# Performance work log

Hardware: AMD Instinct MI355X
Metric: run time of the kernel (lower is better)

## Reference

```python
import jax, jax.numpy as jnp
import numpy as np

H = 512      # hidden_dim
OPS = 12     # num_ops
E = 112      # total_edges = num_cells * sum(i+2 for i in range(num_nodes)) = 8*14


def setup_inputs() -> dict:
    key = jax.random.key(0)
    ks = jax.random.split(key, 16)
    s = lambda k, shape: jax.random.normal(k, shape, dtype=jnp.float32) * 0.05
    return {
        "temperature": 1,
        "h0": s(ks[0], (2, H)),
        "c0": s(ks[1], (2, H)),
        "Wih0": s(ks[2], (4 * H, H)),
        "Whh0": s(ks[3], (4 * H, H)),
        "bih0": s(ks[4], (4 * H,)),
        "bhh0": s(ks[5], (4 * H,)),
        "Wih1": s(ks[6], (4 * H, H)),
        "Whh1": s(ks[7], (4 * H, H)),
        "bih1": s(ks[8], (4 * H,)),
        "bhh1": s(ks[9], (4 * H,)),
        "emb": s(ks[10], (OPS, H)),
        "cW1": s(ks[11], (E, H, H)),
        "cb1": s(ks[12], (E, H)),
        "cW2": s(ks[13], (E, H, OPS)),
        "cb2": s(ks[14], (E, OPS)),
    }


def _lstm_cell(x, h, c, Wih, Whh, bih, bhh):
    # PyTorch LSTM gate order: i, f, g, o
    gates = x @ Wih.T + bih + h @ Whh.T + bhh  # [4H]
    i, f, g, o = jnp.split(gates, 4)
    c2 = jax.nn.sigmoid(f) * c + jax.nn.sigmoid(i) * jnp.tanh(g)
    h2 = jax.nn.sigmoid(o) * jnp.tanh(c2)
    return h2, c2


def reference(temperature, h0, c0, Wih0, Whh0, bih0, bhh0,
              Wih1, Whh1, bih1, bhh1, emb, cW1, cb1, cW2, cb2):
    temp = jnp.asarray(temperature, jnp.float32)
    # Gumbel-max trick == torch Categorical sampling (fixed on-device noise)
    gumbel = jax.random.gumbel(jax.random.key(42), (E, OPS), dtype=jnp.float32)

    def step(carry, xs):
        h, c, prev_action = carry          # h, c: [2, H]
        idx, W1, b1, W2, b2, gnoise = xs
        x = jnp.where(idx == 0, jnp.zeros((H,), jnp.float32), emb[prev_action])
        h0n, c0n = _lstm_cell(x, h[0], c[0], Wih0, Whh0, bih0, bhh0)
        h1n, c1n = _lstm_cell(h0n, h[1], c[1], Wih1, Whh1, bih1, bhh1)
        hmlp = jax.nn.relu(h1n @ W1 + b1)   # controller hidden
        logits = (hmlp @ W2 + b2) / temp    # [OPS]
        logp = jax.nn.log_softmax(logits)
        action = jnp.argmax(logits + gnoise).astype(jnp.int32)
        lp = logp[action]
        ent = -jnp.sum(jnp.exp(logp) * logp)
        new_carry = (jnp.stack([h0n, h1n]), jnp.stack([c0n, c1n]), action)
        return new_carry, (action, lp, ent)

    init = (h0, c0, jnp.int32(0))
    xs = (jnp.arange(E), cW1, cb1, cW2, cb2, gumbel)
    _, (actions, log_probs, entropies) = jax.lax.scan(step, init, xs)
    return actions, log_probs, entropies
```

## Files before the change

### kernel.cpp

```cpp
#include <hip/hip_runtime.h>
#include <math.h>

#define H    512
#define OPS  12
#define E    112
#define NWG  128
#define NT   256

typedef unsigned long long u64;

#define TW_BASE  16
#define TW_HB0   0
#define TW_HB1   1024
#define TW_HMB   2048
#define TW_TOTAL 3072

__device__ __forceinline__ float sigf(float x) { return 1.f / (1.f + expf(-x)); }

__device__ __forceinline__ void threefry_42(unsigned x0, unsigned x1,
                                            unsigned& o0, unsigned& o1) {
  const unsigned k0 = 0u, k1 = 42u;
  const unsigned k2 = k0 ^ k1 ^ 0x1BD11BDAu;
  x0 += k0; x1 += k1;
#define TF_R(rot) { x0 += x1; x1 = (x1 << rot) | (x1 >> (32 - rot)); x1 ^= x0; }
  TF_R(13) TF_R(15) TF_R(26) TF_R(6)
  x0 += k1; x1 += k2 + 1u;
  TF_R(17) TF_R(29) TF_R(16) TF_R(24)
  x0 += k2; x1 += k0 + 2u;
  TF_R(13) TF_R(15) TF_R(26) TF_R(6)
  x0 += k0; x1 += k1 + 3u;
  TF_R(17) TF_R(29) TF_R(16) TF_R(24)
  x0 += k1; x1 += k2 + 4u;
  TF_R(13) TF_R(15) TF_R(26) TF_R(6)
  x0 += k2; x1 += k0 + 5u;
#undef TF_R
  o0 = x0; o1 = x1;
}

__device__ __forceinline__ float bits_to_gumbel(unsigned bits) {
  unsigned fb = (bits >> 9) | 0x3f800000u;
  float u = __uint_as_float(fb) - 1.0f;
  u = u + 1.17549435e-38f;
  u = fmaxf(1.17549435e-38f, u);
  return -logf(-logf(u));
}

__device__ __forceinline__ float decode_temp(const void* temp_p) {
  float tf = *(const float*)temp_p;
  float a = fabsf(tf);
  if (a > 1e-6f && a < 1e6f) return tf;
  int ti = *(const int*)temp_p;
  if (ti != 0 && ti > -1000000 && ti < 1000000) return (float)ti;
  double td = *(const double*)temp_p;
  double ad = fabs(td);
  if (ad > 1e-6 && ad < 1e6) return (float)td;
  return 1.0f;
}

__device__ __forceinline__ void tag_store(u64* p, unsigned tag, float f) {
  u64 v = ((u64)tag << 32) | (u64)__float_as_uint(f);
  __hip_atomic_store(p, v, __ATOMIC_RELAXED, __HIP_MEMORY_SCOPE_SYSTEM);
}
__device__ __forceinline__ float tag_poll(const u64* p, unsigned tag) {
  u64 v = __hip_atomic_load(p, __ATOMIC_RELAXED, __HIP_MEMORY_SCOPE_SYSTEM);
  while ((unsigned)(v >> 32) != tag) {
    __builtin_amdgcn_s_sleep(1);
    v = __hip_atomic_load(p, __ATOMIC_RELAXED, __HIP_MEMORY_SCOPE_SYSTEM);
  }
  return __uint_as_float((unsigned)v);
}

__global__ void k_init(u64* tw) {
  int t = blockIdx.x * blockDim.x + threadIdx.x;
  if (t < TW_TOTAL) tw[t] = 0ull;
}
__global__ void k_diag(float* out, float v) {
  if (threadIdx.x == 0 && blockIdx.x == 0) out[0] = v;
}

__global__ void __launch_bounds__(NT)
policy_persist(const void* temp_p,
               const float* __restrict__ h0_in, const float* __restrict__ c0_in,
               const float* __restrict__ Wih0,  const float* __restrict__ Whh0,
               const float* __restrict__ bih0,  const float* __restrict__ bhh0,
               const float* __restrict__ Wih1,  const float* __restrict__ Whh1,
               const float* __restrict__ bih1,  const float* __restrict__ bhh1,
               const float* __restrict__ emb,   const float* __restrict__ cW1,
               const float* __restrict__ cb1,   const float* __restrict__ cW2,
               const float* __restrict__ cb2,
               float* __restrict__ out, float* ws) {
  __shared__ __align__(16) float shp0[H], shp1[H], hm[H];
  __shared__ float g0pre[16], g1bpre[16], g1loc[16];
  __shared__ float ewloc[12 * 16], b0loc[16], b1loc[16];
  __shared__ float gum[E * OPS];
  __shared__ float w1s[512 * 5];
  __shared__ float w2s[512 * 13];
  __shared__ float c0loc[4], c1loc[4];
  __shared__ float spart[4][4];
  __shared__ int s_act;

  const int tid = threadIdx.x;
  const int bid = blockIdx.x;
  const int j0  = bid * 4;
  const int cb  = (bid & 7) * 16 + (bid >> 3);
  const float invt = 1.f / decode_temp(temp_p);

  u64* HB0 = (u64*)(ws + TW_BASE) + TW_HB0;
  u64* HB1 = (u64*)(ws + TW_BASE) + TW_HB1;
  u64* HMB = (u64*)(ws + TW_BASE) + TW_HMB;

  for (int p = tid; p < E * OPS; p += NT) {
    unsigned y0, y1;
    threefry_42(0u, (unsigned)p, y0, y1);
    gum[p] = bits_to_gumbel(y0 ^ y1);
  }
  for (int j = tid; j < H; j += NT) {
    shp0[j] = h0_in[j];
    shp1[j] = h0_in[H + j];
  }
  if (tid < 192) {
    int a = tid / 16, ridx = tid % 16;
    int g = ridx >> 2, dj = ridx & 3;
    int row = g * H + j0 + dj;
    const float* er = emb + a * H;
    const float* wr = Wih0 + (size_t)row * H;
    float acc = 0.f;
    for (int k = 0; k < H; k += 4) {
      float4 e4 = *(const float4*)(er + k);
      float4 w4 = *(const float4*)(wr + k);
      acc += e4.x * w4.x + e4.y * w4.y + e4.z * w4.z + e4.w * w4.w;
    }
    ewloc[tid] = acc;
  }
  if (tid < 16) {
    int g = tid >> 2, dj = tid & 3;
    int row = g * H + j0 + dj;
    b0loc[tid] = bih0[row] + bhh0[row];
    b1loc[tid] = bih1[row] + bhh1[row];
  }
  if (tid < 4) {
    c0loc[tid] = c0_in[j0 + tid];
    c1loc[tid] = c0_in[H + j0 + tid];
  }
  __syncthreads();

  {
    int rowidx = tid >> 3, lane = tid & 7;
    int cell = rowidx >> 4, ridx = rowidx & 15;
    int g = ridx >> 2, dj = ridx & 3;
    int row = g * H + j0 + dj;
    const float* wr = (cell ? Whh1 : Whh0) + (size_t)row * H + lane * 64;
    const float* hv = (cell ? shp1 : shp0) + lane * 64;
    float acc = 0.f;
#pragma unroll
    for (int k = 0; k < 64; k += 4) {
      float4 w4 = *(const float4*)(wr + k);
      acc += w4.x * hv[k] + w4.y * hv[k + 1] + w4.z * hv[k + 2] + w4.w * hv[k + 3];
    }
    acc += __shfl_xor(acc, 1);
    acc += __shfl_xor(acc, 2);
    acc += __shfl_xor(acc, 4);
    if (lane == 0) {
      if (cell == 0) g0pre[ridx] = acc + b0loc[ridx];
      else           g1bpre[ridx] = acc;
    }
    const float* wb = cW1 + (size_t)cb * 4;
    float4 r0 = *(const float4*)(wb + (size_t)tid * H);
    float4 r1 = *(const float4*)(wb + (size_t)(tid + 256) * H);
    int k0 = tid * 5, k1 = (tid + 256) * 5;
    w1s[k0] = r0.x; w1s[k0 + 1] = r0.y; w1s[k0 + 2] = r0.z; w1s[k0 + 3] = r0.w;
    w1s[k1] = r1.x; w1s[k1 + 1] = r1.y; w1s[k1 + 2] = r1.z; w1s[k1 + 3] = r1.w;
  }
  __syncthreads();

#pragma unroll 1
  for (int i = 0; i < E; ++i) {
    const int p = i & 1;
    const unsigned tg = (unsigned)(i + 1);

    if (i > 0) {
      const int q = (i - 1) & 1;
      const unsigned tgp = (unsigned)i;
      int t2 = tid * 2;
      hm[t2]     = tag_poll(&HMB[q * 512 + t2],     tgp);
      hm[t2 + 1] = tag_poll(&HMB[q * 512 + t2 + 1], tgp);
      __syncthreads();
      if (tid < 64) {
        float lg[OPS];
#pragma unroll
        for (int o = 0; o < OPS; ++o) lg[o] = 0.f;
#pragma unroll
        for (int jj = 0; jj < 8; ++jj) {
          int j = jj * 64 + tid;
          float hmv = hm[j];
          const float* w2r = &w2s[j * 13];
#pragma unroll
          for (int o = 0; o < OPS; ++o) lg[o] += hmv * w2r[o];
        }
#pragma unroll
        for (int s = 1; s < 64; s <<= 1) {
#pragma unroll
          for (int o = 0; o < OPS; ++o) lg[o] += __shfl_xor(lg[o], s);
        }
#pragma unroll
        for (int o = 0; o < OPS; ++o) lg[o] = (lg[o] + cb2[(i - 1) * OPS + o]) * invt;
        float mx = lg[0];
#pragma unroll
        for (int o = 1; o < OPS; ++o) mx = fmaxf(mx, lg[o]);
        float se = 0.f;
#pragma unroll
        for (int o = 0; o < OPS; ++o) se += expf(lg[o] - mx);
        float logZ = mx + logf(se);
        float best = -1e30f; int act = 0;
#pragma unroll
        for (int o = 0; o < OPS; ++o) {
          float v = lg[o] + gum[(i - 1) * OPS + o];
          if (v > best) { best = v; act = o; }
        }
        if (tid == 0) {
          s_act = act;
          if (bid == 0) {
            float lp = lg[act] - logZ;
            float ent = 0.f;
            for (int o = 0; o < OPS; ++o) {
              float l2 = lg[o] - logZ;
              ent -= expf(l2) * l2;
            }
            out[i - 1]         = (float)act;
            out[E + i - 1]     = lp;
            out[2 * E + i - 1] = ent;
          }
        }
      }
    }

    if (tid < 4) {
      int a = (i > 0) ? s_act : -1;
      float gi = g0pre[tid];
      float gf = g0pre[4 + tid];
      float gg = g0pre[8 + tid];
      float go = g0pre[12 + tid];
      if (a >= 0) {
        gi += ewloc[a * 16 + tid];
        gf += ewloc[a * 16 + 4 + tid];
        gg += ewloc[a * 16 + 8 + tid];
        go += ewloc[a * 16 + 12 + tid];
      }
      float cn = sigf(gf) * c0loc[tid] + sigf(gi) * tanhf(gg);
      c0loc[tid] = cn;
      tag_store(&HB0[p * 512 + j0 + tid], tg, sigf(go) * tanhf(cn));
    }

    {
      int t2 = tid * 2;
      shp0[t2]     = tag_poll(&HB0[p * 512 + t2],     tg);
      shp0[t2 + 1] = tag_poll(&HB0[p * 512 + t2 + 1], tg);
    }
    __syncthreads();

    {
      int ridx = tid >> 4, lane = tid & 15;
      int g = ridx >> 2, dj = ridx & 3;
      int row = g * H + j0 + dj;
      const float* wr = Wih1 + (size_t)row * H + lane * 32;
      const float* hv = shp0 + lane * 32;
      float acc = 0.f;
#pragma unroll
      for (int k = 0; k < 32; k += 4) {
        float4 w4 = *(const float4*)(wr + k);
        acc += w4.x * hv[k] + w4.y * hv[k + 1] + w4.z * hv[k + 2] + w4.w * hv[k + 3];
      }
      acc += __shfl_xor(acc, 1);
      acc += __shfl_xor(acc, 2);
      acc += __shfl_xor(acc, 4);
      acc += __shfl_xor(acc, 8);
      if (lane == 0) g1loc[ridx] = acc + g1bpre[ridx] + b1loc[ridx];
    }
    __syncthreads();

    if (tid < 4) {
      float gi = g1loc[tid];
      float gf = g1loc[4 + tid];
      float gg = g1loc[8 + tid];
      float go = g1loc[12 + tid];
      float cn = sigf(gf) * c1loc[tid] + sigf(gi) * tanhf(gg);
      c1loc[tid] = cn;
      tag_store(&HB1[p * 512 + j0 + tid], tg, sigf(go) * tanhf(cn));
    }

    {
      int t2 = tid * 2;
      shp1[t2]     = tag_poll(&HB1[p * 512 + t2],     tg);
      shp1[t2 + 1] = tag_poll(&HB1[p * 512 + t2 + 1], tg);
    }
    __syncthreads();

    {
      int wv = tid >> 6, ln = tid & 63;
      int jl = ln & 3, ks = ln >> 2;
      int kbase = wv * 128 + ks * 8;
      float acc = 0.f;
#pragma unroll
      for (int t = 0; t < 8; ++t) {
        int k = kbase + t;
        acc += shp1[k] * w1s[k * 5 + jl];
      }
      acc += __shfl_xor(acc, 4);
      acc += __shfl_xor(acc, 8);
      acc += __shfl_xor(acc, 16);
      acc += __shfl_xor(acc, 32);
      if (ln < 4) spart[wv][ln] = acc;
    }
    __syncthreads();
    if (tid < 4) {
      float s = spart[0][tid] + spart[1][tid] + spart[2][tid] + spart[3][tid];
      s += cb1[(size_t)i * H + cb * 4 + tid];
      tag_store(&HMB[p * 512 + cb * 4 + tid], tg, fmaxf(s, 0.f));
    }

    {
      const float* wsrc = cW2 + (size_t)i * H * OPS;
#pragma unroll
      for (int r = 0; r < 6; ++r) {
        int q = tid + 256 * r;
        float4 v = *(const float4*)(wsrc + 4 * q);
        int f = 4 * q;
        w2s[(f / 12) * 13 + (f % 12)]             = v.x;
        w2s[((f + 1) / 12) * 13 + ((f + 1) % 12)] = v.y;
        w2s[((f + 2) / 12) * 13 + ((f + 2) % 12)] = v.z;
        w2s[((f + 3) / 12) * 13 + ((f + 3) % 12)] = v.w;
      }
    }
    if (i + 1 < E) {
      const float* wb = cW1 + (size_t)(i + 1) * H * H + (size_t)cb * 4;
      float4 r0 = *(const float4*)(wb + (size_t)tid * H);
      float4 r1 = *(const float4*)(wb + (size_t)(tid + 256) * H);
      {
        int rowidx = tid >> 3, lane = tid & 7;
        int cell = rowidx >> 4, ridx = rowidx & 15;
        int g = ridx >> 2, dj = ridx & 3;
        int row = g * H + j0 + dj;
        const float* wr = (cell ? Whh1 : Whh0) + (size_t)row * H + lane * 64;
        const float* hv = (cell ? shp1 : shp0) + lane * 64;
        float acc = 0.f;
#pragma unroll
        for (int k = 0; k < 64; k += 4) {
          float4 w4 = *(const float4*)(wr + k);
          acc += w4.x * hv[k] + w4.y * hv[k + 1] + w4.z * hv[k + 2] + w4.w * hv[k + 3];
        }
        acc += __shfl_xor(acc, 1);
        acc += __shfl_xor(acc, 2);
        acc += __shfl_xor(acc, 4);
        if (lane == 0) {
          if (cell == 0) g0pre[ridx] = acc + b0loc[ridx];
          else           g1bpre[ridx] = acc;
        }
      }
      int k0 = tid * 5, k1 = (tid + 256) * 5;
      w1s[k0] = r0.x; w1s[k0 + 1] = r0.y; w1s[k0 + 2] = r0.z; w1s[k0 + 3] = r0.w;
      w1s[k1] = r1.x; w1s[k1 + 1] = r1.y; w1s[k1 + 2] = r1.z; w1s[k1 + 3] = r1.w;
    }
    __syncthreads();
  }

  if (bid == 0) {
    const int q = (E - 1) & 1;
    int t2 = tid * 2;
    hm[t2]     = tag_poll(&HMB[q * 512 + t2],     (unsigned)E);
    hm[t2 + 1] = tag_poll(&HMB[q * 512 + t2 + 1], (unsigned)E);
    __syncthreads();
    if (tid < 64) {
      float lg[OPS];
#pragma unroll
      for (int o = 0; o < OPS; ++o) lg[o] = 0.f;
#pragma unroll
      for (int jj = 0; jj < 8; ++jj) {
        int j = jj * 64 + tid;
        float hmv = hm[j];
        const float* w2r = &w2s[j * 13];
#pragma unroll
        for (int o = 0; o < OPS; ++o) lg[o] += hmv * w2r[o];
      }
#pragma unroll
      for (int s = 1; s < 64; s <<= 1) {
#pragma unroll
        for (int o = 0; o < OPS; ++o) lg[o] += __shfl_xor(lg[o], s);
      }
#pragma unroll
      for (int o = 0; o < OPS; ++o) lg[o] = (lg[o] + cb2[(E - 1) * OPS + o]) * invt;
      float mx = lg[0];
#pragma unroll
      for (int o = 1; o < OPS; ++o) mx = fmaxf(mx, lg[o]);
      float se = 0.f;
#pragma unroll
      for (int o = 0; o < OPS; ++o) se += expf(lg[o] - mx);
      float logZ = mx + logf(se);
      float best = -1e30f; int act = 0;
#pragma unroll
      for (int o = 0; o < OPS; ++o) {
        float v = lg[o] + gum[(E - 1) * OPS + o];
        if (v > best) { best = v; act = o; }
      }
      if (tid == 0) {
        float lp = lg[act] - logZ;
        float ent = 0.f;
        for (int o = 0; o < OPS; ++o) {
          float l2 = lg[o] - logZ;
          ent -= expf(l2) * l2;
        }
        out[E - 1]     = (float)act;
        out[2 * E - 1] = lp;
        out[3 * E - 1] = ent;
      }
    }
  }
}

extern "C" void kernel_launch(void* const* d_in, const int* in_sizes, int n_in,
                              void* d_out, int out_size, void* d_ws, size_t ws_size,
                              hipStream_t stream) {
  (void)out_size; (void)ws_size;
  float* out = (float*)d_out;
  float* ws  = (float*)d_ws;

  (void)hipGetLastError();

  static const long long expect[16] = {
      1, 1024, 1024, 1048576, 1048576, 2048, 2048,
      1048576, 1048576, 2048, 2048, 6144,
      29360128, 57344, 688128, 1344 };
  int bad = -1;
  if (n_in != 16) bad = 99;
  else {
    for (int i = 0; i < 16; ++i)
      if ((long long)in_sizes[i] != expect[i]) { bad = i; break; }
  }

  k_init<<<12, 256, 0, stream>>>((u64*)(ws + TW_BASE));
  if (bad >= 0) {
    k_diag<<<1, 64, 0, stream>>>(out, 80000.0f + (float)bad);
    return;
  }

  policy_persist<<<NWG, NT, 0, stream>>>(
      d_in[0],
      (const float*)d_in[1],  (const float*)d_in[2],
      (const float*)d_in[3],  (const float*)d_in[4],
      (const float*)d_in[5],  (const float*)d_in[6],
      (const float*)d_in[7],  (const float*)d_in[8],
      (const float*)d_in[9],  (const float*)d_in[10],
      (const float*)d_in[11], (const float*)d_in[12],
      (const float*)d_in[13], (const float*)d_in[14],
      (const float*)d_in[15],
      out, ws);

  hipError_t e = hipGetLastError();
  if (e != hipSuccess) {
    k_diag<<<1, 64, 0, stream>>>(out, 90000.0f + (float)(int)e);
  }
}
```

Baseline: 1.074 ms.

## Speculate layer-0 LSTM output for all actions to remove a grid barrier per step

Layer 0 of the LSTM now runs one step ahead and speculatively for all 12 possible previous actions. Each block publishes 12 candidate h0 slices, gathers the full speculative h0 vectors, and precomputes the Wih1 contributions for every action. Once the sampled action is known, the matching h0, c0 and layer-1 input term are picked, which removes one global tag-polled exchange (HB0) from the serial critical path of each step. In exchange it does 12x the layer-0 gate and Wih1 work, polls a 12x larger exchange buffer, and uses much more shared memory. It also merges the paired tag polls into a single loop.

Result: slower. 3.097 ms (+188.4%).

```diff
diff --git a/kernel.cpp b/kernel.cpp
--- a/kernel.cpp
+++ b/kernel.cpp
@@ -9,11 +9,10 @@
 
 typedef unsigned long long u64;
 
-#define TW_BASE  16
-#define TW_HB0   0
-#define TW_HB1   1024
-#define TW_HMB   2048
-#define TW_TOTAL 3072
+#define TW_HB1   0
+#define TW_HMB   1024
+#define TW_SPEC  2048
+#define TW_TOTAL (2048 + 2 * 6144)
 
 __device__ __forceinline__ float sigf(float x) { return 1.f / (1.f + expf(-x)); }
 
@@ -61,13 +60,17 @@
   u64 v = ((u64)tag << 32) | (u64)__float_as_uint(f);
   __hip_atomic_store(p, v, __ATOMIC_RELAXED, __HIP_MEMORY_SCOPE_SYSTEM);
 }
-__device__ __forceinline__ float tag_poll(const u64* p, unsigned tag) {
-  u64 v = __hip_atomic_load(p, __ATOMIC_RELAXED, __HIP_MEMORY_SCOPE_SYSTEM);
-  while ((unsigned)(v >> 32) != tag) {
+__device__ __forceinline__ void tag_poll2(const u64* p0, const u64* p1,
+                                          unsigned tag, float& f0, float& f1) {
+  u64 a = __hip_atomic_load(p0, __ATOMIC_RELAXED, __HIP_MEMORY_SCOPE_SYSTEM);
+  u64 b = __hip_atomic_load(p1, __ATOMIC_RELAXED, __HIP_MEMORY_SCOPE_SYSTEM);
+  while (((unsigned)(a >> 32) != tag) || ((unsigned)(b >> 32) != tag)) {
     __builtin_amdgcn_s_sleep(1);
-    v = __hip_atomic_load(p, __ATOMIC_RELAXED, __HIP_MEMORY_SCOPE_SYSTEM);
-  }
-  return __uint_as_float((unsigned)v);
+    a = __hip_atomic_load(p0, __ATOMIC_RELAXED, __HIP_MEMORY_SCOPE_SYSTEM);
+    b = __hip_atomic_load(p1, __ATOMIC_RELAXED, __HIP_MEMORY_SCOPE_SYSTEM);
+  }
+  f0 = __uint_as_float((unsigned)a);
+  f1 = __uint_as_float((unsigned)b);
 }
 
 __global__ void k_init(u64* tw) {
@@ -89,8 +92,10 @@
                const float* __restrict__ cb1,   const float* __restrict__ cW2,
                const float* __restrict__ cb2,
                float* __restrict__ out, float* ws) {
-  __shared__ __align__(16) float shp0[H], shp1[H], hm[H];
+  __shared__ __align__(16) float h0full[H], shp1[H], hm[H];
+  __shared__ __align__(16) float h0specfull[12 * H];
   __shared__ float g0pre[16], g1bpre[16], g1loc[16];
+  __shared__ float G1Aspec[12 * 16], c0spec[12 * 4];
   __shared__ float ewloc[12 * 16], b0loc[16], b1loc[16];
   __shared__ float gum[E * OPS];
   __shared__ float w1s[512 * 5];
@@ -105,9 +110,9 @@
   const int cb  = (bid & 7) * 16 + (bid >> 3);
   const float invt = 1.f / decode_temp(temp_p);
 
-  u64* HB0 = (u64*)(ws + TW_BASE) + TW_HB0;
-  u64* HB1 = (u64*)(ws + TW_BASE) + TW_HB1;
-  u64* HMB = (u64*)(ws + TW_BASE) + TW_HMB;
+  u64* HB1  = (u64*)(ws + 16) + TW_HB1;
+  u64* HMB  = (u64*)(ws + 16) + TW_HMB;
+  u64* SPEC = (u64*)(ws + 16) + TW_SPEC;
 
   for (int p = tid; p < E * OPS; p += NT) {
     unsigned y0, y1;
@@ -115,8 +120,8 @@
     gum[p] = bits_to_gumbel(y0 ^ y1);
   }
   for (int j = tid; j < H; j += NT) {
-    shp0[j] = h0_in[j];
-    shp1[j] = h0_in[H + j];
+    h0full[j] = h0_in[j];
+    shp1[j]   = h0_in[H + j];
   }
   if (tid < 192) {
     int a = tid / 16, ridx = tid % 16;
@@ -150,7 +155,7 @@
     int g = ridx >> 2, dj = ridx & 3;
     int row = g * H + j0 + dj;
     const float* wr = (cell ? Whh1 : Whh0) + (size_t)row * H + lane * 64;
-    const float* hv = (cell ? shp1 : shp0) + lane * 64;
+    const float* hv = (cell ? shp1 : h0full) + lane * 64;
     float acc = 0.f;
 #pragma unroll
     for (int k = 0; k < 64; k += 4) {
@@ -173,17 +178,51 @@
   }
   __syncthreads();
 
+  if (tid < 4) {
+    float gi = g0pre[tid];
+    float gf = g0pre[4 + tid];
+    float gg = g0pre[8 + tid];
+    float go = g0pre[12 + tid];
+    float cn = sigf(gf) * c0loc[tid] + sigf(gi) * tanhf(gg);
+    c0loc[tid] = cn;
+    tag_store(&SPEC[j0 + tid], 1u, sigf(go) * tanhf(cn));
+  }
+  {
+    int t2 = tid * 2;
+    tag_poll2(&SPEC[t2], &SPEC[t2 + 1], 1u, h0full[t2], h0full[t2 + 1]);
+  }
+  __syncthreads();
+  {
+    int ridx = tid >> 4, lane = tid & 15;
+    int g = ridx >> 2, dj = ridx & 3;
+    int row = g * H + j0 + dj;
+    const float* wr = Wih1 + (size_t)row * H + lane * 32;
+    const float* hv = h0full + lane * 32;
+    float acc = 0.f;
+#pragma unroll
+    for (int k = 0; k < 32; k += 4) {
+      float4 w4 = *(const float4*)(wr + k);
+      acc += w4.x * hv[k] + w4.y * hv[k + 1] + w4.z * hv[k + 2] + w4.w * hv[k + 3];
+    }
+    acc += __shfl_xor(acc, 1);
+    acc += __shfl_xor(acc, 2);
+    acc += __shfl_xor(acc, 4);
+    acc += __shfl_xor(acc, 8);
+    if (lane == 0) G1Aspec[ridx] = acc;
+  }
+  __syncthreads();
+
 #pragma unroll 1
   for (int i = 0; i < E; ++i) {
     const int p = i & 1;
     const unsigned tg = (unsigned)(i + 1);
+    int a = 0;
 
     if (i > 0) {
       const int q = (i - 1) & 1;
-      const unsigned tgp = (unsigned)i;
       int t2 = tid * 2;
-      hm[t2]     = tag_poll(&HMB[q * 512 + t2],     tgp);
-      hm[t2 + 1] = tag_poll(&HMB[q * 512 + t2 + 1], tgp);
+      tag_poll2(&HMB[q * 512 + t2], &HMB[q * 512 + t2 + 1], (unsigned)i,
+                hm[t2], hm[t2 + 1]);
       __syncthreads();
       if (tid < 64) {
         float lg[OPS];
@@ -232,52 +271,14 @@
           }
         }
       }
-    }
-
-    if (tid < 4) {
-      int a = (i > 0) ? s_act : -1;
-      float gi = g0pre[tid];
-      float gf = g0pre[4 + tid];
-      float gg = g0pre[8 + tid];
-      float go = g0pre[12 + tid];
-      if (a >= 0) {
-        gi += ewloc[a * 16 + tid];
-        gf += ewloc[a * 16 + 4 + tid];
-        gg += ewloc[a * 16 + 8 + tid];
-        go += ewloc[a * 16 + 12 + tid];
-      }
-      float cn = sigf(gf) * c0loc[tid] + sigf(gi) * tanhf(gg);
-      c0loc[tid] = cn;
-      tag_store(&HB0[p * 512 + j0 + tid], tg, sigf(go) * tanhf(cn));
-    }
-
-    {
-      int t2 = tid * 2;
-      shp0[t2]     = tag_poll(&HB0[p * 512 + t2],     tg);
-      shp0[t2 + 1] = tag_poll(&HB0[p * 512 + t2 + 1], tg);
-    }
-    __syncthreads();
-
-    {
-      int ridx = tid >> 4, lane = tid & 15;
-      int g = ridx >> 2, dj = ridx & 3;
-      int row = g * H + j0 + dj;
-      const float* wr = Wih1 + (size_t)row * H + lane * 32;
-      const float* hv = shp0 + lane * 32;
-      float acc = 0.f;
-#pragma unroll
-      for (int k = 0; k < 32; k += 4) {
-        float4 w4 = *(const float4*)(wr + k);
-        acc += w4.x * hv[k] + w4.y * hv[k + 1] + w4.z * hv[k + 2] + w4.w * hv[k + 3];
-      }
-      acc += __shfl_xor(acc, 1);
-      acc += __shfl_xor(acc, 2);
-      acc += __shfl_xor(acc, 4);
-      acc += __shfl_xor(acc, 8);
-      if (lane == 0) g1loc[ridx] = acc + g1bpre[ridx] + b1loc[ridx];
-    }
-    __syncthreads();
-
+      __syncthreads();
+      a = s_act;
+      if (tid < 4) c0loc[tid] = c0spec[a * 4 + tid];
+      for (int j = tid; j < H; j += NT) h0full[j] = h0specfull[a * 512 + j];
+      __syncthreads();
+    }
+
+    if (tid < 16) g1loc[tid] = G1Aspec[a * 16 + tid] + g1bpre[tid] + b1loc[tid];
     if (tid < 4) {
       float gi = g1loc[tid];
       float gf = g1loc[4 + tid];
@@ -288,36 +289,23 @@
       tag_store(&HB1[p * 512 + j0 + tid], tg, sigf(go) * tanhf(cn));
     }
 
-    {
-      int t2 = tid * 2;
-      shp1[t2]     = tag_poll(&HB1[p * 512 + t2],     tg);
-      shp1[t2 + 1] = tag_poll(&HB1[p * 512 + t2 + 1], tg);
-    }
-    __syncthreads();
-
-    {
-      int wv = tid >> 6, ln = tid & 63;
-      int jl = ln & 3, ks = ln >> 2;
-      int kbase = wv * 128 + ks * 8;
+    if (tid < 128) {
+      int ridx = tid >> 3, lane = tid & 7;
+      int g = ridx >> 2, dj = ridx & 3;
+      int row = g * H + j0 + dj;
+      const float* wr = Whh0 + (size_t)row * H + lane * 64;
+      const float* hv = h0full + lane * 64;
       float acc = 0.f;
 #pragma unroll
-      for (int t = 0; t < 8; ++t) {
-        int k = kbase + t;
-        acc += shp1[k] * w1s[k * 5 + jl];
-      }
+      for (int k = 0; k < 64; k += 4) {
+        float4 w4 = *(const float4*)(wr + k);
+        acc += w4.x * hv[k] + w4.y * hv[k + 1] + w4.z * hv[k + 2] + w4.w * hv[k + 3];
+      }
+      acc += __shfl_xor(acc, 1);
+      acc += __shfl_xor(acc, 2);
       acc += __shfl_xor(acc, 4);
-      acc += __shfl_xor(acc, 8);
-      acc += __shfl_xor(acc, 16);
-      acc += __shfl_xor(acc, 32);
-      if (ln < 4) spart[wv][ln] = acc;
-    }
-    __syncthreads();
-    if (tid < 4) {
-      float s = spart[0][tid] + spart[1][tid] + spart[2][tid] + spart[3][tid];
-      s += cb1[(size_t)i * H + cb * 4 + tid];
-      tag_store(&HMB[p * 512 + cb * 4 + tid], tg, fmaxf(s, 0.f));
-    }
-
+      if (lane == 0) g0pre[ridx] = acc + b0loc[ridx];
+    }
     {
       const float* wsrc = cW2 + (size_t)i * H * OPS;
 #pragma unroll
@@ -331,17 +319,49 @@
         w2s[((f + 3) / 12) * 13 + ((f + 3) % 12)] = v.w;
       }
     }
+
+    {
+      int t2 = tid * 2;
+      tag_poll2(&HB1[p * 512 + t2], &HB1[p * 512 + t2 + 1], tg,
+                shp1[t2], shp1[t2 + 1]);
+    }
+    __syncthreads();
+
+    {
+      int wv = tid >> 6, ln = tid & 63;
+      int jl = ln & 3, ks = ln >> 2;
+      int kbase = wv * 128 + ks * 8;
+      float acc = 0.f;
+#pragma unroll
+      for (int t = 0; t < 8; ++t) {
+        int k = kbase + t;
+        acc += shp1[k] * w1s[k * 5 + jl];
+      }
+      acc += __shfl_xor(acc, 4);
+      acc += __shfl_xor(acc, 8);
+      acc += __shfl_xor(acc, 16);
+      acc += __shfl_xor(acc, 32);
+      if (ln < 4) spart[wv][ln] = acc;
+    }
+    __syncthreads();
+    if (tid < 4) {
+      float s = spart[0][tid] + spart[1][tid] + spart[2][tid] + spart[3][tid];
+      s += cb1[(size_t)i * H + cb * 4 + tid];
+      tag_store(&HMB[p * 512 + cb * 4 + tid], tg, fmaxf(s, 0.f));
+    }
+
     if (i + 1 < E) {
+      const int pn = (i + 1) & 1;
+      const unsigned tgn = (unsigned)(i + 2);
       const float* wb = cW1 + (size_t)(i + 1) * H * H + (size_t)cb * 4;
       float4 r0 = *(const float4*)(wb + (size_t)tid * H);
       float4 r1 = *(const float4*)(wb + (size_t)(tid + 256) * H);
-      {
-        int rowidx = tid >> 3, lane = tid & 7;
-        int cell = rowidx >> 4, ridx = rowidx & 15;
+      if (tid < 128) {
+        int ridx = tid >> 3, lane = tid & 7;
         int g = ridx >> 2, dj = ridx & 3;
         int row = g * H + j0 + dj;
-        const float* wr = (cell ? Whh1 : Whh0) + (size_t)row * H + lane * 64;
-        const float* hv = (cell ? shp1 : shp0) + lane * 64;
+        const float* wr = Whh1 + (size_t)row * H + lane * 64;
+        const float* hv = shp1 + lane * 64;
         float acc = 0.f;
 #pragma unroll
         for (int k = 0; k < 64; k += 4) {
@@ -351,14 +371,77 @@
         acc += __shfl_xor(acc, 1);
         acc += __shfl_xor(acc, 2);
         acc += __shfl_xor(acc, 4);
-        if (lane == 0) {
-          if (cell == 0) g0pre[ridx] = acc + b0loc[ridx];
-          else           g1bpre[ridx] = acc;
-        }
-      }
-      int k0 = tid * 5, k1 = (tid + 256) * 5;
-      w1s[k0] = r0.x; w1s[k0 + 1] = r0.y; w1s[k0 + 2] = r0.z; w1s[k0 + 3] = r0.w;
-      w1s[k1] = r1.x; w1s[k1 + 1] = r1.y; w1s[k1 + 2] = r1.z; w1s[k1 + 3] = r1.w;
+        if (lane == 0) g1bpre[ridx] = acc;
+      }
+      if (tid < 48) {
+        int aa = tid >> 2, col = tid & 3;
+        float gi = g0pre[col]      + ewloc[aa * 16 + col];
+        float gf = g0pre[4 + col]  + ewloc[aa * 16 + 4 + col];
+        float gg = g0pre[8 + col]  + ewloc[aa * 16 + 8 + col];
+        float go = g0pre[12 + col] + ewloc[aa * 16 + 12 + col];
+        float cn = sigf(gf) * c0loc[col] + sigf(gi) * tanhf(gg);
+        c0spec[aa * 4 + col] = cn;
+        tag_store(&SPEC[pn * 6144 + aa * 512 + j0 + col], tgn,
+                  sigf(go) * tanhf(cn));
+      }
+      {
+        int k0 = tid * 5, k1 = (tid + 256) * 5;
+        w1s[k0] = r0.x; w1s[k0 + 1] = r0.y; w1s[k0 + 2] = r0.z; w1s[k0 + 3] = r0.w;
+        w1s[k1] = r1.x; w1s[k1 + 1] = r1.y; w1s[k1 + 2] = r1.z; w1s[k1 + 3] = r1.w;
+      }
+      {
+        const u64* sp = &SPEC[pn * 6144];
+        const int base = tid * 24;
+        u64 v[24];
+        bool ok;
+        do {
+          ok = true;
+#pragma unroll
+          for (int r = 0; r < 24; ++r)
+            v[r] = __hip_atomic_load(&sp[base + r], __ATOMIC_RELAXED,
+                                     __HIP_MEMORY_SCOPE_SYSTEM);
+#pragma unroll
+          for (int r = 0; r < 24; ++r)
+            if ((unsigned)(v[r] >> 32) != tgn) ok = false;
+          if (!ok) __builtin_amdgcn_s_sleep(1);
+        } while (!ok);
+#pragma unroll
+        for (int r = 0; r < 24; ++r)
+          h0specfull[base + r] = __uint_as_float((unsigned)v[r]);
+      }
+      __syncthreads();
+      {
+        int ridx = tid >> 4, lane = tid & 15;
+        int g = ridx >> 2, dj = ridx & 3;
+        int row = g * H + j0 + dj;
+        const float* wr = Wih1 + (size_t)row * H + lane * 32;
+        float4 w0 = *(const float4*)(wr);
+        float4 w1 = *(const float4*)(wr + 4);
+        float4 w2 = *(const float4*)(wr + 8);
+        float4 w3 = *(const float4*)(wr + 12);
+        float4 w4 = *(const float4*)(wr + 16);
+        float4 w5 = *(const float4*)(wr + 20);
+        float4 w6 = *(const float4*)(wr + 24);
+        float4 w7 = *(const float4*)(wr + 28);
+#pragma unroll 1
+        for (int aa = 0; aa < 12; ++aa) {
+          const float* hv = &h0specfull[aa * 512 + lane * 32];
+          float acc = 0.f;
+          acc += w0.x * hv[0]  + w0.y * hv[1]  + w0.z * hv[2]  + w0.w * hv[3];
+          acc += w1.x * hv[4]  + w1.y * hv[5]  + w1.z * hv[6]  + w1.w * hv[7];
+          acc += w2.x * hv[8]  + w2.y * hv[9]  + w2.z * hv[10] + w2.w * hv[11];
+          acc += w3.x * hv[12] + w3.y * hv[13] + w3.z * hv[14] + w3.w * hv[15];
+          acc += w4.x * hv[16] + w4.y * hv[17] + w4.z * hv[18] + w4.w * hv[19];
+          acc += w5.x * hv[20] + w5.y * hv[21] + w5.z * hv[22] + w5.w * hv[23];
+          acc += w6.x * hv[24] + w6.y * hv[25] + w6.z * hv[26] + w6.w * hv[27];
+          acc += w7.x * hv[28] + w7.y * hv[29] + w7.z * hv[30] + w7.w * hv[31];
+          acc += __shfl_xor(acc, 1);
+          acc += __shfl_xor(acc, 2);
+          acc += __shfl_xor(acc, 4);
+          acc += __shfl_xor(acc, 8);
+          if (lane == 0) G1Aspec[aa * 16 + ridx] = acc;
+        }
+      }
     }
     __syncthreads();
   }
@@ -366,8 +449,8 @@
   if (bid == 0) {
     const int q = (E - 1) & 1;
     int t2 = tid * 2;
-    hm[t2]     = tag_poll(&HMB[q * 512 + t2],     (unsigned)E);
-    hm[t2 + 1] = tag_poll(&HMB[q * 512 + t2 + 1], (unsigned)E);
+    tag_poll2(&HMB[q * 512 + t2], &HMB[q * 512 + t2 + 1], (unsigned)E,
+              hm[t2], hm[t2 + 1]);
     __syncthreads();
     if (tid < 64) {
       float lg[OPS];
@@ -436,7 +519,7 @@
       if ((long long)in_sizes[i] != expect[i]) { bad = i; break; }
   }
 
-  k_init<<<12, 256, 0, stream>>>((u64*)(ws + TW_BASE));
+  k_init<<<56, 256, 0, stream>>>((u64*)(ws + 16));
   if (bad >= 0) {
     k_diag<<<1, 64, 0, stream>>>(out, 80000.0f + (float)bad);
     return;
```

## Shrink persistent grid to 32 workgroups with 16 columns each and pre-transposed W1

Applied to the files above, without the earlier changes.

Cuts the persistent kernel from 128 to 32 workgroups, so each one owns 16 hidden columns instead of 4. This reduces how many agents take part in the cross-workgroup tag polling each step. When the workspace is large enough, a separate kernel first re-lays out the 112 cW1 matrices into per-workgroup contiguous tiles so the per-step W1 loads are coalesced. It also restructures the recurrent Whh0/Whh1 products across the step, and polls two flags together in one loop. In exchange, each workgroup does four times the per-step GEMV work, and an extra full pass over the large cW1 tensor is added before the main kernel.

Measured after the change: 2.234 ms. +108.0%, slower.

```diff
diff --git a/kernel.cpp b/kernel.cpp
--- a/kernel.cpp
+++ b/kernel.cpp
@@ -4,16 +4,17 @@
 #define H    512
 #define OPS  12
 #define E    112
-#define NWG  128
+#define NWG  32
 #define NT   256
+#define JW   16
 
 typedef unsigned long long u64;
 
-#define TW_BASE  16
 #define TW_HB0   0
 #define TW_HB1   1024
 #define TW_HMB   2048
 #define TW_TOTAL 3072
+#define WS_W1T_F (16 + 2 * TW_TOTAL)
 
 __device__ __forceinline__ float sigf(float x) { return 1.f / (1.f + expf(-x)); }
 
@@ -61,13 +62,17 @@
   u64 v = ((u64)tag << 32) | (u64)__float_as_uint(f);
   __hip_atomic_store(p, v, __ATOMIC_RELAXED, __HIP_MEMORY_SCOPE_SYSTEM);
 }
-__device__ __forceinline__ float tag_poll(const u64* p, unsigned tag) {
-  u64 v = __hip_atomic_load(p, __ATOMIC_RELAXED, __HIP_MEMORY_SCOPE_SYSTEM);
-  while ((unsigned)(v >> 32) != tag) {
+__device__ __forceinline__ void tag_poll2(const u64* p0, const u64* p1,
+                                          unsigned tag, float& f0, float& f1) {
+  u64 a = __hip_atomic_load(p0, __ATOMIC_RELAXED, __HIP_MEMORY_SCOPE_SYSTEM);
+  u64 b = __hip_atomic_load(p1, __ATOMIC_RELAXED, __HIP_MEMORY_SCOPE_SYSTEM);
+  while (((unsigned)(a >> 32) != tag) || ((unsigned)(b >> 32) != tag)) {
     __builtin_amdgcn_s_sleep(1);
-    v = __hip_atomic_load(p, __ATOMIC_RELAXED, __HIP_MEMORY_SCOPE_SYSTEM);
-  }
-  return __uint_as_float((unsigned)v);
+    a = __hip_atomic_load(p0, __ATOMIC_RELAXED, __HIP_MEMORY_SCOPE_SYSTEM);
+    b = __hip_atomic_load(p1, __ATOMIC_RELAXED, __HIP_MEMORY_SCOPE_SYSTEM);
+  }
+  f0 = __uint_as_float((unsigned)a);
+  f1 = __uint_as_float((unsigned)b);
 }
 
 __global__ void k_init(u64* tw) {
@@ -76,6 +81,19 @@
 }
 __global__ void k_diag(float* out, float v) {
   if (threadIdx.x == 0 && blockIdx.x == 0) out[0] = v;
+}
+
+__global__ void __launch_bounds__(NT)
+k_w1t(const float* __restrict__ cW1, float* __restrict__ w1t) {
+  int t = blockIdx.x * NT + threadIdx.x;
+  size_t e0 = (size_t)t * 4;
+  int i = (int)(e0 >> 18);
+  int rem = (int)(e0 & 262143);
+  int k = rem >> 9, j = rem & 511;
+  int b = j >> 4, jc = j & 15;
+  float4 v = *(const float4*)(cW1 + e0);
+  size_t dst = (((size_t)(i * 32 + b) * 512 + k) << 4) + jc;
+  *(float4*)(w1t + dst) = v;
 }
 
 __global__ void __launch_bounds__(NT)
@@ -88,26 +106,26 @@
                const float* __restrict__ emb,   const float* __restrict__ cW1,
                const float* __restrict__ cb1,   const float* __restrict__ cW2,
                const float* __restrict__ cb2,
-               float* __restrict__ out, float* ws) {
-  __shared__ __align__(16) float shp0[H], shp1[H], hm[H];
-  __shared__ float g0pre[16], g1bpre[16], g1loc[16];
-  __shared__ float ewloc[12 * 16], b0loc[16], b1loc[16];
+               float* __restrict__ out, float* ws, int use_w1t) {
+  __shared__ __align__(16) float h0full[H], shp1[H], hm[H];
+  __shared__ float g0pre[64], g1bpre[64], g1loc[64];
+  __shared__ float ewloc[12 * 64], b0loc[64], b1loc[64];
   __shared__ float gum[E * OPS];
-  __shared__ float w1s[512 * 5];
+  __shared__ __align__(16) float w1s[512 * 17];
   __shared__ float w2s[512 * 13];
-  __shared__ float c0loc[4], c1loc[4];
+  __shared__ float c0loc[JW], c1loc[JW];
   __shared__ float spart[4][4];
   __shared__ int s_act;
 
   const int tid = threadIdx.x;
   const int bid = blockIdx.x;
-  const int j0  = bid * 4;
-  const int cb  = (bid & 7) * 16 + (bid >> 3);
+  const int j0  = bid * JW;
   const float invt = 1.f / decode_temp(temp_p);
 
-  u64* HB0 = (u64*)(ws + TW_BASE) + TW_HB0;
-  u64* HB1 = (u64*)(ws + TW_BASE) + TW_HB1;
-  u64* HMB = (u64*)(ws + TW_BASE) + TW_HMB;
+  u64* HB0 = (u64*)(ws + 16) + TW_HB0;
+  u64* HB1 = (u64*)(ws + 16) + TW_HB1;
+  u64* HMB = (u64*)(ws + 16) + TW_HMB;
+  const float* W1T = ws + WS_W1T_F;
 
   for (int p = tid; p < E * OPS; p += NT) {
     unsigned y0, y1;
@@ -115,12 +133,12 @@
     gum[p] = bits_to_gumbel(y0 ^ y1);
   }
   for (int j = tid; j < H; j += NT) {
-    shp0[j] = h0_in[j];
-    shp1[j] = h0_in[H + j];
-  }
-  if (tid < 192) {
-    int a = tid / 16, ridx = tid % 16;
-    int g = ridx >> 2, dj = ridx & 3;
+    h0full[j] = h0_in[j];
+    shp1[j]   = h0_in[H + j];
+  }
+  for (int e = tid; e < 12 * 64; e += NT) {
+    int a = e >> 6, ridx = e & 63;
+    int g = ridx >> 4, dj = ridx & 15;
     int row = g * H + j0 + dj;
     const float* er = emb + a * H;
     const float* wr = Wih0 + (size_t)row * H;
@@ -130,27 +148,29 @@
       float4 w4 = *(const float4*)(wr + k);
       acc += e4.x * w4.x + e4.y * w4.y + e4.z * w4.z + e4.w * w4.w;
     }
-    ewloc[tid] = acc;
-  }
-  if (tid < 16) {
-    int g = tid >> 2, dj = tid & 3;
+    ewloc[e] = acc;
+  }
+  if (tid < 64) {
+    int g = tid >> 4, dj = tid & 15;
     int row = g * H + j0 + dj;
     b0loc[tid] = bih0[row] + bhh0[row];
     b1loc[tid] = bih1[row] + bhh1[row];
   }
-  if (tid < 4) {
+  if (tid < JW) {
     c0loc[tid] = c0_in[j0 + tid];
     c1loc[tid] = c0_in[H + j0 + tid];
   }
   __syncthreads();
 
-  {
-    int rowidx = tid >> 3, lane = tid & 7;
-    int cell = rowidx >> 4, ridx = rowidx & 15;
-    int g = ridx >> 2, dj = ridx & 3;
+#pragma unroll 1
+  for (int it = 0; it < 4; ++it) {
+    int task = it * NT + tid;
+    int rowidx = task >> 3, lane = task & 7;
+    int cell = rowidx >> 6, ridx = rowidx & 63;
+    int g = ridx >> 4, dj = ridx & 15;
     int row = g * H + j0 + dj;
     const float* wr = (cell ? Whh1 : Whh0) + (size_t)row * H + lane * 64;
-    const float* hv = (cell ? shp1 : shp0) + lane * 64;
+    const float* hv = (cell ? shp1 : h0full) + lane * 64;
     float acc = 0.f;
 #pragma unroll
     for (int k = 0; k < 64; k += 4) {
@@ -164,12 +184,26 @@
       if (cell == 0) g0pre[ridx] = acc + b0loc[ridx];
       else           g1bpre[ridx] = acc;
     }
-    const float* wb = cW1 + (size_t)cb * 4;
-    float4 r0 = *(const float4*)(wb + (size_t)tid * H);
-    float4 r1 = *(const float4*)(wb + (size_t)(tid + 256) * H);
-    int k0 = tid * 5, k1 = (tid + 256) * 5;
-    w1s[k0] = r0.x; w1s[k0 + 1] = r0.y; w1s[k0 + 2] = r0.z; w1s[k0 + 3] = r0.w;
-    w1s[k1] = r1.x; w1s[k1 + 1] = r1.y; w1s[k1 + 2] = r1.z; w1s[k1 + 3] = r1.w;
+  }
+  if (use_w1t) {
+    const float* wt = W1T + ((size_t)bid * 512 << 4);
+#pragma unroll
+    for (int r = 0; r < 8; ++r) {
+      int q = r * NT + tid;
+      float4 v = *(const float4*)(wt + (size_t)q * 4);
+      int k = q >> 2, jc0 = (q & 3) * 4;
+      float* d = &w1s[k * 17 + jc0];
+      d[0] = v.x; d[1] = v.y; d[2] = v.z; d[3] = v.w;
+    }
+  } else {
+#pragma unroll
+    for (int r = 0; r < 8; ++r) {
+      int q = r * NT + tid;
+      int k = q >> 2, jc0 = (q & 3) * 4;
+      float4 v = *(const float4*)(cW1 + (size_t)k * H + j0 + jc0);
+      float* d = &w1s[k * 17 + jc0];
+      d[0] = v.x; d[1] = v.y; d[2] = v.z; d[3] = v.w;
+    }
   }
   __syncthreads();
 
@@ -177,13 +211,13 @@
   for (int i = 0; i < E; ++i) {
     const int p = i & 1;
     const unsigned tg = (unsigned)(i + 1);
+    int a = -1;
 
     if (i > 0) {
       const int q = (i - 1) & 1;
-      const unsigned tgp = (unsigned)i;
       int t2 = tid * 2;
-      hm[t2]     = tag_poll(&HMB[q * 512 + t2],     tgp);
-      hm[t2 + 1] = tag_poll(&HMB[q * 512 + t2 + 1], tgp);
+      tag_poll2(&HMB[q * 512 + t2], &HMB[q * 512 + t2 + 1], (unsigned)i,
+                hm[t2], hm[t2 + 1]);
       __syncthreads();
       if (tid < 64) {
         float lg[OPS];
@@ -232,19 +266,20 @@
           }
         }
       }
-    }
-
-    if (tid < 4) {
-      int a = (i > 0) ? s_act : -1;
+      __syncthreads();
+      a = s_act;
+    }
+
+    if (tid < JW) {
       float gi = g0pre[tid];
-      float gf = g0pre[4 + tid];
-      float gg = g0pre[8 + tid];
-      float go = g0pre[12 + tid];
+      float gf = g0pre[16 + tid];
+      float gg = g0pre[32 + tid];
+      float go = g0pre[48 + tid];
       if (a >= 0) {
-        gi += ewloc[a * 16 + tid];
-        gf += ewloc[a * 16 + 4 + tid];
-        gg += ewloc[a * 16 + 8 + tid];
-        go += ewloc[a * 16 + 12 + tid];
+        gi += ewloc[a * 64 + tid];
+        gf += ewloc[a * 64 + 16 + tid];
+        gg += ewloc[a * 64 + 32 + tid];
+        go += ewloc[a * 64 + 48 + tid];
       }
       float cn = sigf(gf) * c0loc[tid] + sigf(gi) * tanhf(gg);
       c0loc[tid] = cn;
@@ -253,17 +288,19 @@
 
     {
       int t2 = tid * 2;
-      shp0[t2]     = tag_poll(&HB0[p * 512 + t2],     tg);
-      shp0[t2 + 1] = tag_poll(&HB0[p * 512 + t2 + 1], tg);
+      tag_poll2(&HB0[p * 512 + t2], &HB0[p * 512 + t2 + 1], tg,
+                h0full[t2], h0full[t2 + 1]);
     }
     __syncthreads();
 
-    {
-      int ridx = tid >> 4, lane = tid & 15;
-      int g = ridx >> 2, dj = ridx & 3;
+#pragma unroll 1
+    for (int it = 0; it < 4; ++it) {
+      int task = it * NT + tid;
+      int ridx = task >> 4, lane = task & 15;
+      int g = ridx >> 4, dj = ridx & 15;
       int row = g * H + j0 + dj;
       const float* wr = Wih1 + (size_t)row * H + lane * 32;
-      const float* hv = shp0 + lane * 32;
+      const float* hv = h0full + lane * 32;
       float acc = 0.f;
 #pragma unroll
       for (int k = 0; k < 32; k += 4) {
@@ -278,46 +315,35 @@
     }
     __syncthreads();
 
-    if (tid < 4) {
+    if (tid < JW) {
       float gi = g1loc[tid];
-      float gf = g1loc[4 + tid];
-      float gg = g1loc[8 + tid];
-      float go = g1loc[12 + tid];
+      float gf = g1loc[16 + tid];
+      float gg = g1loc[32 + tid];
+      float go = g1loc[48 + tid];
       float cn = sigf(gf) * c1loc[tid] + sigf(gi) * tanhf(gg);
       c1loc[tid] = cn;
       tag_store(&HB1[p * 512 + j0 + tid], tg, sigf(go) * tanhf(cn));
     }
 
-    {
-      int t2 = tid * 2;
-      shp1[t2]     = tag_poll(&HB1[p * 512 + t2],     tg);
-      shp1[t2 + 1] = tag_poll(&HB1[p * 512 + t2 + 1], tg);
-    }
-    __syncthreads();
-
-    {
-      int wv = tid >> 6, ln = tid & 63;
-      int jl = ln & 3, ks = ln >> 2;
-      int kbase = wv * 128 + ks * 8;
+#pragma unroll 1
+    for (int it = 0; it < 2; ++it) {
+      int task = it * NT + tid;
+      int ridx = task >> 3, lane = task & 7;
+      int g = ridx >> 4, dj = ridx & 15;
+      int row = g * H + j0 + dj;
+      const float* wr = Whh0 + (size_t)row * H + lane * 64;
+      const float* hv = h0full + lane * 64;
       float acc = 0.f;
 #pragma unroll
-      for (int t = 0; t < 8; ++t) {
-        int k = kbase + t;
-        acc += shp1[k] * w1s[k * 5 + jl];
-      }
+      for (int k = 0; k < 64; k += 4) {
+        float4 w4 = *(const float4*)(wr + k);
+        acc += w4.x * hv[k] + w4.y * hv[k + 1] + w4.z * hv[k + 2] + w4.w * hv[k + 3];
+      }
+      acc += __shfl_xor(acc, 1);
+      acc += __shfl_xor(acc, 2);
       acc += __shfl_xor(acc, 4);
-      acc += __shfl_xor(acc, 8);
-      acc += __shfl_xor(acc, 16);
-      acc += __shfl_xor(acc, 32);
-      if (ln < 4) spart[wv][ln] = acc;
-    }
-    __syncthreads();
-    if (tid < 4) {
-      float s = spart[0][tid] + spart[1][tid] + spart[2][tid] + spart[3][tid];
-      s += cb1[(size_t)i * H + cb * 4 + tid];
-      tag_store(&HMB[p * 512 + cb * 4 + tid], tg, fmaxf(s, 0.f));
-    }
-
+      if (lane == 0) g0pre[ridx] = acc + b0loc[ridx];
+    }
     {
       const float* wsrc = cW2 + (size_t)i * H * OPS;
 #pragma unroll
@@ -331,17 +357,67 @@
         w2s[((f + 3) / 12) * 13 + ((f + 3) % 12)] = v.w;
       }
     }
+
+    {
+      int t2 = tid * 2;
+      tag_poll2(&HB1[p * 512 + t2], &HB1[p * 512 + t2 + 1], tg,
+                shp1[t2], shp1[t2 + 1]);
+    }
+    __syncthreads();
+
+#pragma unroll 1
+    for (int cg = 0; cg < 4; ++cg) {
+      {
+        int wv = tid >> 6, ln = tid & 63;
+        int jl = ln & 3, ks = ln >> 2;
+        int kbase = wv * 128 + ks * 8;
+        float acc = 0.f;
+#pragma unroll
+        for (int t = 0; t < 8; ++t) {
+          int k = kbase + t;
+          acc += shp1[k] * w1s[k * 17 + cg * 4 + jl];
+        }
+        acc += __shfl_xor(acc, 4);
+        acc += __shfl_xor(acc, 8);
+        acc += __shfl_xor(acc, 16);
+        acc += __shfl_xor(acc, 32);
+        if (ln < 4) spart[wv][ln] = acc;
+      }
+      __syncthreads();
+      if (tid < 4) {
+        float s = spart[0][tid] + spart[1][tid] + spart[2][tid] + spart[3][tid];
+        s += cb1[(size_t)i * H + j0 + cg * 4 + tid];
+        tag_store(&HMB[p * 512 + j0 + cg * 4 + tid], tg, fmaxf(s, 0.f));
+      }
+      __syncthreads();
+    }
+
     if (i + 1 < E) {
-      const float* wb = cW1 + (size_t)(i + 1) * H * H + (size_t)cb * 4;
-      float4 r0 = *(const float4*)(wb + (size_t)tid * H);
-      float4 r1 = *(const float4*)(wb + (size_t)(tid + 256) * H);
-      {
-        int rowidx = tid >> 3, lane = tid & 7;
-        int cell = rowidx >> 4, ridx = rowidx & 15;
-        int g = ridx >> 2, dj = ridx & 3;
+      float4 v[8];
+      if (use_w1t) {
+        const float* wt = W1T + ((size_t)((i + 1) * 32 + bid) * 512 << 4);
+#pragma unroll
+        for (int r = 0; r < 8; ++r) {
+          int q = r * NT + tid;
+          v[r] = *(const float4*)(wt + (size_t)q * 4);
+        }
+      } else {
+        const float* wb = cW1 + (size_t)(i + 1) * H * H;
+#pragma unroll
+        for (int r = 0; r < 8; ++r) {
+          int q = r * NT + tid;
+          int k = q >> 2, jc0 = (q & 3) * 4;
+          v[r] = *(const float4*)(wb + (size_t)k * H + j0 + jc0);
+        }
+      }
+#pragma unroll 1
+      for (int it = 0; it < 2; ++it) {
+        int task = it * NT + tid;
+        int ridx = task >> 3, lane = task & 7;
+        int g = ridx >> 4, dj = ridx & 15;
         int row = g * H + j0 + dj;
-        const float* wr = (cell ? Whh1 : Whh0) + (size_t)row * H + lane * 64;
-        const float* hv = (cell ? shp1 : shp0) + lane * 64;
+        const float* wr = Whh1 + (size_t)row * H + lane * 64;
+        const float* hv = shp1 + lane * 64;
         float acc = 0.f;
 #pragma unroll
         for (int k = 0; k < 64; k += 4) {
@@ -351,14 +427,15 @@
         acc += __shfl_xor(acc, 1);
         acc += __shfl_xor(acc, 2);
         acc += __shfl_xor(acc, 4);
-        if (lane == 0) {
-          if (cell == 0) g0pre[ridx] = acc + b0loc[ridx];
-          else           g1bpre[ridx] = acc;
-        }
-      }
-      int k0 = tid * 5, k1 = (tid + 256) * 5;
-      w1s[k0] = r0.x; w1s[k0 + 1] = r0.y; w1s[k0 + 2] = r0.z; w1s[k0 + 3] = r0.w;
-      w1s[k1] = r1.x; w1s[k1 + 1] = r1.y; w1s[k1 + 2] = r1.z; w1s[k1 + 3] = r1.w;
+        if (lane == 0) g1bpre[ridx] = acc;
+      }
+#pragma unroll
+      for (int r = 0; r < 8; ++r) {
+        int q = r * NT + tid;
+        int k = q >> 2, jc0 = (q & 3) * 4;
+        float* d = &w1s[k * 17 + jc0];
+        d[0] = v[r].x; d[1] = v[r].y; d[2] = v[r].z; d[3] = v[r].w;
+      }
     }
     __syncthreads();
   }
@@ -366,8 +443,8 @@
   if (bid == 0) {
     const int q = (E - 1) & 1;
     int t2 = tid * 2;
-    hm[t2]     = tag_poll(&HMB[q * 512 + t2],     (unsigned)E);
-    hm[t2 + 1] = tag_poll(&HMB[q * 512 + t2 + 1], (unsigned)E);
+    tag_poll2(&HMB[q * 512 + t2], &HMB[q * 512 + t2 + 1], (unsigned)E,
+              hm[t2], hm[t2 + 1]);
     __syncthreads();
     if (tid < 64) {
       float lg[OPS];
@@ -419,7 +496,7 @@
 extern "C" void kernel_launch(void* const* d_in, const int* in_sizes, int n_in,
                               void* d_out, int out_size, void* d_ws, size_t ws_size,
                               hipStream_t stream) {
-  (void)out_size; (void)ws_size;
+  (void)out_size;
   float* out = (float*)d_out;
   float* ws  = (float*)d_ws;
 
@@ -436,10 +513,16 @@
       if ((long long)in_sizes[i] != expect[i]) { bad = i; break; }
   }
 
-  k_init<<<12, 256, 0, stream>>>((u64*)(ws + TW_BASE));
+  k_init<<<12, 256, 0, stream>>>((u64*)(ws + 16));
   if (bad >= 0) {
     k_diag<<<1, 64, 0, stream>>>(out, 80000.0f + (float)bad);
     return;
+  }
+
+  const size_t need = (size_t)WS_W1T_F * 4 + (size_t)29360128 * 4;
+  int use_w1t = (ws_size >= need) ? 1 : 0;
+  if (use_w1t) {
+    k_w1t<<<28672, 256, 0, stream>>>((const float*)d_in[12], ws + WS_W1T_F);
   }
 
   policy_persist<<<NWG, NT, 0, stream>>>(
@@ -452,7 +535,7 @@
       (const float*)d_in[11], (const float*)d_in[12],
       (const float*)d_in[13], (const float*)d_in[14],
       (const float*)d_in[15],
-      out, ws);
+      out, ws, use_w1t);
 
   hipError_t e = hipGetLastError();
   if (e != hipSuccess) {
```
